# Optimization experiments

Hardware: AMD Instinct MI355X
Metric: run time of the kernel (lower is better)

The kernel has to match this reference:

```python
import jax, jax.numpy as jnp
import numpy as np

NEG_SLOPE = 0.2  # LeakyReLU slope used in the torch module


def setup_inputs() -> dict:
    key = jax.random.key(0)
    k1, k2, k3, k4 = jax.random.split(key, 4)
    B, W, K, E = 32, 128, 128, 256  # E = 2*window_size (gatv2 doubles embed_dim)
    x = jax.random.normal(k1, (B, W, K), dtype=jnp.float32)
    lin_w = jax.random.normal(k2, (E, 2 * W), dtype=jnp.float32) * 0.05
    lin_b = jnp.zeros((E,), dtype=jnp.float32)
    a = jax.random.normal(k3, (E, 1), dtype=jnp.float32) * 0.1
    bias = jax.random.normal(k4, (K, K), dtype=jnp.float32) * 0.1
    return {"x": x, "lin_w": lin_w, "lin_b": lin_b, "a": a, "bias": bias}


def reference(x, lin_w, lin_b, a, bias):
    # x: [B, window, K] -> permute to [B, K, window]
    xp = jnp.transpose(x, (0, 2, 1))
    Wd = xp.shape[-1]
    # lin(concat(v_i, v_j)) = v_i @ Wl^T + v_j @ Wr^T + b, avoiding the
    # explicit repeat_interleave/repeat/cat of the torch code (same math).
    Wl, Wr = lin_w[:, :Wd], lin_w[:, Wd:]
    left = jnp.einsum('bkw,ew->bke', xp, Wl)   # [B, K, E]
    right = jnp.einsum('bkw,ew->bke', xp, Wr)  # [B, K, E]
    h = left[:, :, None, :] + right[:, None, :, :] + lin_b  # [B, K, K, E]
    h = jnp.where(h >= 0, h, NEG_SLOPE * h)  # LeakyReLU(0.2)
    e = jnp.einsum('bije,eo->bij', h, a)     # matmul with a, squeeze -> [B, K, K]
    e = e + bias                             # use_bias=True
    att = jax.nn.softmax(e, axis=2)          # dropout=0 / eval -> identity
    out = jax.nn.sigmoid(jnp.einsum('bij,bjw->biw', att, xp))  # [B, K, W]
    return jnp.transpose(out, (0, 2, 1))     # [B, window, K]
```

## Files before the change

### kernel.cpp

```cpp
#include <hip/hip_runtime.h>


typedef float v2f __attribute__((ext_vector_type(2)));
typedef float v4f __attribute__((ext_vector_type(4)));
typedef short bf16x8 __attribute__((ext_vector_type(8)));

#define WS_A6  2097152
#define WS_A4  (2097152 + 256)

__device__ __forceinline__ unsigned pack_bf16x2(float a, float b) {
    unsigned ua = __builtin_bit_cast(unsigned, a);
    unsigned ub = __builtin_bit_cast(unsigned, b);
    ua = (ua + 0x7FFFu + ((ua >> 16) & 1u)) >> 16;
    ub = (ub + 0x7FFFu + ((ub >> 16) & 1u)) >> 16;
    return ua | (ub << 16);
}

__global__ __launch_bounds__(256) void k_linear(
    const float* __restrict__ x, const float* __restrict__ lin_w,
    const float* __restrict__ lin_b, const float* __restrict__ a,
    float* __restrict__ ws)
{
    __shared__ unsigned short xT[128 * 136];
    __shared__ unsigned short As[64 * 136];

    const int t = threadIdx.x;
    const int b = blockIdx.x, rt = blockIdx.y;
    const bool isL = (rt < 4);

    if (b == 0 && rt == 0) {
        float av = a[t];
        ws[WS_A6 + t] = 0.6f * av;
        ws[WS_A4 + t] = 0.4f * av;
    }

    {
        const float* xg = x + b * 16384;
        #pragma unroll
        for (int q = 0; q < 8; ++q) {
            const int idx = t + q * 256;
            const int wp = idx >> 5;
            const int k4 = (idx & 31) << 2;
            const v4f r0 = *(const v4f*)(xg + (2 * wp) * 128 + k4);
            const v4f r1 = *(const v4f*)(xg + (2 * wp + 1) * 128 + k4);
            const int g   = wp >> 2;
            const int off = (2 * wp) & 7;
            #pragma unroll
            for (int u = 0; u < 4; ++u) {
                const int k = k4 + u;
                const int gs = g ^ ((k >> 3) & 15);
                *(unsigned*)&xT[k * 136 + (gs << 3) + off] = pack_bf16x2(r0[u], r1[u]);
            }
        }
    }
    {
        #pragma unroll
        for (int q = 0; q < 16; ++q) {
            const int idx = t + q * 256;
            const int rr = idx >> 6, wp2 = idx & 63;
            const int r = rt * 64 + rr;
            const float* Ag = isL ? (lin_w + (size_t)r * 256)
                                  : (lin_w + (size_t)(r - 256) * 256 + 128);
            const v2f wv = *(const v2f*)(Ag + 2 * wp2);
            *(unsigned*)&As[rr * 136 + 2 * wp2] = pack_bf16x2(wv.x, wv.y);
        }
    }
    __syncthreads();

    const int l = t & 63, wave = t >> 6;
    const int m0 = wave * 16;
    const int lr = l & 15, lg = l >> 4;

    bf16x8 af[4];
    #pragma unroll
    for (int kc = 0; kc < 4; ++kc)
        af[kc] = *(const bf16x8*)&As[(m0 + lr) * 136 + kc * 32 + lg * 8];

    v4f acc[8];
    #pragma unroll
    for (int nf = 0; nf < 8; ++nf) acc[nf] = (v4f){0.f, 0.f, 0.f, 0.f};

    #pragma unroll
    for (int nf = 0; nf < 8; ++nf) {
        const int row = nf * 16 + lr;
        const int vr = (row >> 3) & 15;
        #pragma unroll
        for (int kc = 0; kc < 4; ++kc) {
            const int g = kc * 4 + lg;
            const bf16x8 bfv = *(const bf16x8*)&xT[row * 136 + ((g ^ vr) << 3)];
            acc[nf] = __builtin_amdgcn_mfma_f32_16x16x32_bf16(af[kc], bfv, acc[nf], 0, 0, 0);
        }
    }

    const int rb = rt * 64 + m0 + lg * 4;
    #pragma unroll
    for (int j = 0; j < 4; ++j) {
        const float lb = isL ? lin_b[rb + j] : 0.f;
        float* dst = ws + (size_t)(b * 512 + rb + j) * 128;
        #pragma unroll
        for (int nf = 0; nf < 8; ++nf)
            dst[nf * 16 + lr] = acc[nf][j] + lb;
    }
}

__global__ __launch_bounds__(256, 1) void k_attn(
    const float* __restrict__ x, const float* __restrict__ bias,
    const float* __restrict__ ws, float* __restrict__ out)
{
    __shared__ float Rs[2][8192];
    __shared__ float Lt[256 * 16];
    __shared__ float att[16 * 132];
    __shared__ float as6[256], as4[256];

    const int t = threadIdx.x;
    const int b = blockIdx.x, it = blockIdx.y;
    const float* Pb = ws + (size_t)b * 65536;
    const float* Rsrc = Pb + 32768;

    v4f rx[8];
#define RLOAD(n_) do { const float* s_ = Rsrc + (n_) * 8192 + t * 4;  \
    _Pragma("unroll") for (int q = 0; q < 8; ++q)                     \
      rx[q] = *(const v4f*)(s_ + q * 1024); } while (0)

    RLOAD(0);

    {
        const float* Ls = Pb + it * 16;
        #pragma unroll
        for (int q = 0; q < 4; ++q) {
            const int idx = t + q * 256;
            const int e = idx >> 2, il4 = (idx & 3) * 4;
            *(v4f*)&Lt[e * 16 + il4] = *(const v4f*)(Ls + e * 128 + il4);
        }
    }
    as6[t] = ws[WS_A6 + t];
    as4[t] = ws[WS_A4 + t];

    const int jp = t & 31, iq = t >> 5;
    const int j0 = jp * 4, il0 = iq * 2;

    float acc0[4] = {}, acc1[4] = {};
    float dr[4] = {};
    float dl0 = 0.f, dl1 = 0.f;

    #pragma unroll 1
    for (int n = 0; n < 4; ++n) {
        float* rs = &Rs[n & 1][0];
        {
            float* d_ = rs + t * 4;
            #pragma unroll
            for (int q = 0; q < 8; ++q) *(v4f*)(d_ + q * 1024) = rx[q];
        }
        if (n < 3) RLOAD(n + 1);
        __syncthreads();

        const int eg0 = n * 64;
        #pragma unroll
        for (int g = 0; g < 16; ++g) {
            const int e0 = g * 4, eg = eg0 + e0;
            v4f rv[4]; float2 lv[4];
            #pragma unroll
            for (int u = 0; u < 4; ++u) {
                rv[u] = *(const v4f*)&rs[(e0 + u) * 128 + j0];
                lv[u] = *(const float2*)&Lt[(eg + u) * 16 + il0];
            }
            const v4f a6v = *(const v4f*)&as6[eg];
            const v4f a4v = *(const v4f*)&as4[eg];
            #pragma unroll
            for (int u = 0; u < 4; ++u) {
                const float a6u = a6v[u], a4u = a4v[u];
                const float l0 = lv[u].x, l1 = lv[u].y;
                dl0 = fmaf(a6u, l0, dl0);
                dl1 = fmaf(a6u, l1, dl1);
                #pragma unroll
                for (int jj = 0; jj < 4; ++jj) {
                    const float r = rv[u][jj];
                    dr[jj]   = fmaf(a6u, r, dr[jj]);
                    acc0[jj] = fmaf(a4u, fabsf(l0 + r), acc0[jj]);
                    acc1[jj] = fmaf(a4u, fabsf(l1 + r), acc1[jj]);
                }
            }
        }
    }
    __syncthreads();

    float* xT = &Rs[0][0];
    {
        const float* xg = x + b * 16384;
        #pragma unroll
        for (int q = 0; q < 16; ++q) {
            const int idx = t + q * 256;
            const int w = idx >> 5, j4 = (idx & 31) * 4;
            const int s = ((j4 >> 2) & 15) << 1;
            const v4f xv = *(const v4f*)(xg + w * 128 + j4);
            xT[(j4 + 0) * 128 + (w ^ s)] = xv[0];
            xT[(j4 + 1) * 128 + (w ^ s)] = xv[1];
            xT[(j4 + 2) * 128 + (w ^ s)] = xv[2];
            xT[(j4 + 3) * 128 + (w ^ s)] = xv[3];
        }
    }

    const int i0r = it * 16 + il0;
    float ev0[4], ev1[4];
    {
        const v4f b0 = *(const v4f*)(bias + (i0r + 0) * 128 + j0);
        const v4f b1 = *(const v4f*)(bias + (i0r + 1) * 128 + j0);
        #pragma unroll
        for (int jj = 0; jj < 4; ++jj) {
            ev0[jj] = acc0[jj] + dl0 + dr[jj] + b0[jj];
            ev1[jj] = acc1[jj] + dl1 + dr[jj] + b1[jj];
        }
    }
#define SOFTMAX_ROW(EV, ROW) do {                                               \
    float m_ = fmaxf(fmaxf(EV[0], EV[1]), fmaxf(EV[2], EV[3]));                 \
    _Pragma("unroll") for (int d_ = 1; d_ <= 16; d_ <<= 1)                      \
        m_ = fmaxf(m_, __shfl_xor(m_, d_));                                     \
    float p0 = __expf(EV[0] - m_), p1 = __expf(EV[1] - m_);                     \
    float p2 = __expf(EV[2] - m_), p3 = __expf(EV[3] - m_);                     \
    float s_ = p0 + p1 + p2 + p3;                                               \
    _Pragma("unroll") for (int d_ = 1; d_ <= 16; d_ <<= 1)                      \
        s_ += __shfl_xor(s_, d_);                                               \
    const float inv_ = 1.f / s_;                                                \
    *(v4f*)&att[(ROW) * 132 + j0] =                                             \
        (v4f){p0 * inv_, p1 * inv_, p2 * inv_, p3 * inv_}; } while (0)

    SOFTMAX_ROW(ev0, il0 + 0);
    SOFTMAX_ROW(ev1, il0 + 1);
    __syncthreads();

    const int iq2 = t & 3, wp = t >> 2;
    const int i4 = iq2 * 4, w0 = wp * 2;
    float o[2][4] = {};
    #pragma unroll 4
    for (int jc = 0; jc < 32; ++jc) {
        const int wx = w0 ^ ((jc & 15) << 1);
        v4f av[4]; v2f xv[4];
        #pragma unroll
        for (int q = 0; q < 4; ++q)
            av[q] = *(const v4f*)&att[(i4 + q) * 132 + jc * 4];
        #pragma unroll
        for (int u = 0; u < 4; ++u)
            xv[u] = *(const v2f*)&xT[(jc * 4 + u) * 128 + wx];
        #pragma unroll
        for (int u = 0; u < 4; ++u)
            #pragma unroll
            for (int q = 0; q < 4; ++q) {
                o[0][q] = fmaf(xv[u].x, av[q][u], o[0][q]);
                o[1][q] = fmaf(xv[u].y, av[q][u], o[1][q]);
            }
    }
    #pragma unroll
    for (int w = 0; w < 2; ++w) {
        v4f r;
        r[0] = 1.f / (1.f + __expf(-o[w][0]));
        r[1] = 1.f / (1.f + __expf(-o[w][1]));
        r[2] = 1.f / (1.f + __expf(-o[w][2]));
        r[3] = 1.f / (1.f + __expf(-o[w][3]));
        *(v4f*)(out + (size_t)b * 16384 + (w0 + w) * 128 + it * 16 + i4) = r;
    }
}

extern "C" void kernel_launch(void* const* d_in, const int* in_sizes, int n_in,
                              void* d_out, int out_size, void* d_ws, size_t ws_size,
                              hipStream_t stream) {
    const float* x     = (const float*)d_in[0];
    const float* lin_w = (const float*)d_in[1];
    const float* lin_b = (const float*)d_in[2];
    const float* a     = (const float*)d_in[3];
    const float* bias  = (const float*)d_in[4];
    float* ws  = (float*)d_ws;
    float* out = (float*)d_out;

    k_linear<<<dim3(32, 8), 256, 0, stream>>>(x, lin_w, lin_b, a, ws);
    k_attn  <<<dim3(32, 8), 256, 0, stream>>>(x, bias, ws, out);
}
```

Measured before the change: 33.68 us.

## Fuse linear projection into attention kernel, recomputing projections per block in LDS

New measurement: 36.77 us. 1.09x slower.

```diff
diff --git a/kernel.cpp b/kernel.cpp
--- a/kernel.cpp
+++ b/kernel.cpp
@@ -4,9 +4,6 @@
 typedef float v2f __attribute__((ext_vector_type(2)));
 typedef float v4f __attribute__((ext_vector_type(4)));
 typedef short bf16x8 __attribute__((ext_vector_type(8)));
-
-#define WS_A6  2097152
-#define WS_A4  (2097152 + 256)
 
 __device__ __forceinline__ unsigned pack_bf16x2(float a, float b) {
     unsigned ua = __builtin_bit_cast(unsigned, a);
@@ -15,24 +12,25 @@
     ub = (ub + 0x7FFFu + ((ub >> 16) & 1u)) >> 16;
     return ua | (ub << 16);
 }
-
-__global__ __launch_bounds__(256) void k_linear(
+__device__ __forceinline__ float bf2f(unsigned h) {
+    unsigned u = h << 16;
+    return __builtin_bit_cast(float, u);
+}
+
+__global__ __launch_bounds__(256) void k_fused(
     const float* __restrict__ x, const float* __restrict__ lin_w,
     const float* __restrict__ lin_b, const float* __restrict__ a,
-    float* __restrict__ ws)
+    const float* __restrict__ bias, float* __restrict__ out)
 {
     __shared__ unsigned short xT[128 * 136];
-    __shared__ unsigned short As[64 * 136];
+    __shared__ unsigned short As2[64 * 264];
+    __shared__ float Rs[64 * 132];
+    __shared__ float Lt[256 * 18];
+    __shared__ float att[16 * 132];
+    __shared__ float as6[256], as4[256];
 
     const int t = threadIdx.x;
-    const int b = blockIdx.x, rt = blockIdx.y;
-    const bool isL = (rt < 4);
-
-    if (b == 0 && rt == 0) {
-        float av = a[t];
-        ws[WS_A6 + t] = 0.6f * av;
-        ws[WS_A4 + t] = 0.4f * av;
-    }
+    const int b = blockIdx.x, it = blockIdx.y;
 
     {
         const float* xg = x + b * 16384;
@@ -53,89 +51,11 @@
             }
         }
     }
-    {
-        #pragma unroll
-        for (int q = 0; q < 16; ++q) {
-            const int idx = t + q * 256;
-            const int rr = idx >> 6, wp2 = idx & 63;
-            const int r = rt * 64 + rr;
-            const float* Ag = isL ? (lin_w + (size_t)r * 256)
-                                  : (lin_w + (size_t)(r - 256) * 256 + 128);
-            const v2f wv = *(const v2f*)(Ag + 2 * wp2);
-            *(unsigned*)&As[rr * 136 + 2 * wp2] = pack_bf16x2(wv.x, wv.y);
-        }
-    }
-    __syncthreads();
+    as6[t] = 0.6f * a[t];
+    as4[t] = 0.4f * a[t];
 
     const int l = t & 63, wave = t >> 6;
-    const int m0 = wave * 16;
     const int lr = l & 15, lg = l >> 4;
-
-    bf16x8 af[4];
-    #pragma unroll
-    for (int kc = 0; kc < 4; ++kc)
-        af[kc] = *(const bf16x8*)&As[(m0 + lr) * 136 + kc * 32 + lg * 8];
-
-    v4f acc[8];
-    #pragma unroll
-    for (int nf = 0; nf < 8; ++nf) acc[nf] = (v4f){0.f, 0.f, 0.f, 0.f};
-
-    #pragma unroll
-    for (int nf = 0; nf < 8; ++nf) {
-        const int row = nf * 16 + lr;
-        const int vr = (row >> 3) & 15;
-        #pragma unroll
-        for (int kc = 0; kc < 4; ++kc) {
-            const int g = kc * 4 + lg;
-            const bf16x8 bfv = *(const bf16x8*)&xT[row * 136 + ((g ^ vr) << 3)];
-            acc[nf] = __builtin_amdgcn_mfma_f32_16x16x32_bf16(af[kc], bfv, acc[nf], 0, 0, 0);
-        }
-    }
-
-    const int rb = rt * 64 + m0 + lg * 4;
-    #pragma unroll
-    for (int j = 0; j < 4; ++j) {
-        const float lb = isL ? lin_b[rb + j] : 0.f;
-        float* dst = ws + (size_t)(b * 512 + rb + j) * 128;
-        #pragma unroll
-        for (int nf = 0; nf < 8; ++nf)
-            dst[nf * 16 + lr] = acc[nf][j] + lb;
-    }
-}
-
-__global__ __launch_bounds__(256, 1) void k_attn(
-    const float* __restrict__ x, const float* __restrict__ bias,
-    const float* __restrict__ ws, float* __restrict__ out)
-{
-    __shared__ float Rs[2][8192];
-    __shared__ float Lt[256 * 16];
-    __shared__ float att[16 * 132];
-    __shared__ float as6[256], as4[256];
-
-    const int t = threadIdx.x;
-    const int b = blockIdx.x, it = blockIdx.y;
-    const float* Pb = ws + (size_t)b * 65536;
-    const float* Rsrc = Pb + 32768;
-
-    v4f rx[8];
-#define RLOAD(n_) do { const float* s_ = Rsrc + (n_) * 8192 + t * 4;  \
-    _Pragma("unroll") for (int q = 0; q < 8; ++q)                     \
-      rx[q] = *(const v4f*)(s_ + q * 1024); } while (0)
-
-    RLOAD(0);
-
-    {
-        const float* Ls = Pb + it * 16;
-        #pragma unroll
-        for (int q = 0; q < 4; ++q) {
-            const int idx = t + q * 256;
-            const int e = idx >> 2, il4 = (idx & 3) * 4;
-            *(v4f*)&Lt[e * 16 + il4] = *(const v4f*)(Ls + e * 128 + il4);
-        }
-    }
-    as6[t] = ws[WS_A6 + t];
-    as4[t] = ws[WS_A4 + t];
-
     const int jp = t & 31, iq = t >> 5;
     const int j0 = jp * 4, il0 = iq * 2;
 
@@ -144,25 +64,66 @@
     float dl0 = 0.f, dl1 = 0.f;
 
     #pragma unroll 1
-    for (int n = 0; n < 4; ++n) {
-        float* rs = &Rs[n & 1][0];
+    for (int c = 0; c < 4; ++c) {
+        #pragma unroll
+        for (int q = 0; q < 32; ++q) {
+            const int idx = t + q * 256;
+            const int rr = idx >> 7, cp = idx & 127;
+            const v2f wv = *(const v2f*)(lin_w + (size_t)(c * 64 + rr) * 256 + 2 * cp);
+            *(unsigned*)&As2[rr * 264 + 2 * cp] = pack_bf16x2(wv.x, wv.y);
+        }
+        __syncthreads();
+
         {
-            float* d_ = rs + t * 4;
-            #pragma unroll
-            for (int q = 0; q < 8; ++q) *(v4f*)(d_ + q * 1024) = rx[q];
-        }
-        if (n < 3) RLOAD(n + 1);
+            bf16x8 afL[4], afR[4];
+            #pragma unroll
+            for (int kc = 0; kc < 4; ++kc) {
+                afL[kc] = *(const bf16x8*)&As2[(wave * 16 + lr) * 264 + kc * 32 + lg * 8];
+                afR[kc] = *(const bf16x8*)&As2[(wave * 16 + lr) * 264 + 128 + kc * 32 + lg * 8];
+            }
+            v4f accL = (v4f){0.f, 0.f, 0.f, 0.f};
+            {
+                const int row = it * 16 + lr;
+                const int vr = (row >> 3) & 15;
+                #pragma unroll
+                for (int kc = 0; kc < 4; ++kc) {
+                    const bf16x8 bfv = *(const bf16x8*)&xT[row * 136 + (((kc * 4 + lg) ^ vr) << 3)];
+                    accL = __builtin_amdgcn_mfma_f32_16x16x32_bf16(afL[kc], bfv, accL, 0, 0, 0);
+                }
+            }
+            v4f accR[8];
+            #pragma unroll
+            for (int nf = 0; nf < 8; ++nf) accR[nf] = (v4f){0.f, 0.f, 0.f, 0.f};
+            #pragma unroll
+            for (int nf = 0; nf < 8; ++nf) {
+                const int row = nf * 16 + lr;
+                const int vr = (row >> 3) & 15;
+                #pragma unroll
+                for (int kc = 0; kc < 4; ++kc) {
+                    const bf16x8 bfv = *(const bf16x8*)&xT[row * 136 + (((kc * 4 + lg) ^ vr) << 3)];
+                    accR[nf] = __builtin_amdgcn_mfma_f32_16x16x32_bf16(afR[kc], bfv, accR[nf], 0, 0, 0);
+                }
+            }
+            const int el = wave * 16 + lg * 4;
+            #pragma unroll
+            for (int j = 0; j < 4; ++j) {
+                Lt[(c * 64 + el + j) * 18 + lr] = accL[j] + lin_b[c * 64 + el + j];
+                #pragma unroll
+                for (int nf = 0; nf < 8; ++nf)
+                    Rs[(el + j) * 132 + nf * 16 + lr] = accR[nf][j];
+            }
+        }
         __syncthreads();
 
-        const int eg0 = n * 64;
+        const int eg0 = c * 64;
         #pragma unroll
         for (int g = 0; g < 16; ++g) {
             const int e0 = g * 4, eg = eg0 + e0;
             v4f rv[4]; float2 lv[4];
             #pragma unroll
             for (int u = 0; u < 4; ++u) {
-                rv[u] = *(const v4f*)&rs[(e0 + u) * 128 + j0];
-                lv[u] = *(const float2*)&Lt[(eg + u) * 16 + il0];
+                rv[u] = *(const v4f*)&Rs[(e0 + u) * 132 + j0];
+                lv[u] = *(const float2*)&Lt[(eg + u) * 18 + il0];
             }
             const v4f a6v = *(const v4f*)&as6[eg];
             const v4f a4v = *(const v4f*)&as4[eg];
@@ -181,23 +142,7 @@
                 }
             }
         }
-    }
-    __syncthreads();
-
-    float* xT = &Rs[0][0];
-    {
-        const float* xg = x + b * 16384;
-        #pragma unroll
-        for (int q = 0; q < 16; ++q) {
-            const int idx = t + q * 256;
-            const int w = idx >> 5, j4 = (idx & 31) * 4;
-            const int s = ((j4 >> 2) & 15) << 1;
-            const v4f xv = *(const v4f*)(xg + w * 128 + j4);
-            xT[(j4 + 0) * 128 + (w ^ s)] = xv[0];
-            xT[(j4 + 1) * 128 + (w ^ s)] = xv[1];
-            xT[(j4 + 2) * 128 + (w ^ s)] = xv[2];
-            xT[(j4 + 3) * 128 + (w ^ s)] = xv[3];
-        }
+        __syncthreads();
     }
 
     const int i0r = it * 16 + il0;
@@ -230,23 +175,29 @@
 
     const int iq2 = t & 3, wp = t >> 2;
     const int i4 = iq2 * 4, w0 = wp * 2;
+    const int g2 = w0 >> 3, off2 = w0 & 7;
     float o[2][4] = {};
     #pragma unroll 4
     for (int jc = 0; jc < 32; ++jc) {
-        const int wx = w0 ^ ((jc & 15) << 1);
-        v4f av[4]; v2f xv[4];
+        v4f av[4];
         #pragma unroll
         for (int q = 0; q < 4; ++q)
             av[q] = *(const v4f*)&att[(i4 + q) * 132 + jc * 4];
+        float xv0[4], xv1[4];
+        #pragma unroll
+        for (int u = 0; u < 4; ++u) {
+            const int k = jc * 4 + u;
+            const int gs = g2 ^ ((k >> 3) & 15);
+            const unsigned pp = *(const unsigned*)&xT[k * 136 + (gs << 3) + off2];
+            xv0[u] = bf2f(pp & 0xFFFFu);
+            xv1[u] = bf2f(pp >> 16);
+        }
         #pragma unroll
         for (int u = 0; u < 4; ++u)
-            xv[u] = *(const v2f*)&xT[(jc * 4 + u) * 128 + wx];
-        #pragma unroll
-        for (int u = 0; u < 4; ++u)
             #pragma unroll
             for (int q = 0; q < 4; ++q) {
-                o[0][q] = fmaf(xv[u].x, av[q][u], o[0][q]);
-                o[1][q] = fmaf(xv[u].y, av[q][u], o[1][q]);
+                o[0][q] = fmaf(xv0[u], av[q][u], o[0][q]);
+                o[1][q] = fmaf(xv1[u], av[q][u], o[1][q]);
             }
     }
     #pragma unroll
@@ -268,9 +219,8 @@
     const float* lin_b = (const float*)d_in[2];
     const float* a     = (const float*)d_in[3];
     const float* bias  = (const float*)d_in[4];
-    float* ws  = (float*)d_ws;
     float* out = (float*)d_out;
-
-    k_linear<<<dim3(32, 8), 256, 0, stream>>>(x, lin_w, lin_b, a, ws);
-    k_attn  <<<dim3(32, 8), 256, 0, stream>>>(x, bias, ws, out);
-}
+    (void)d_ws; (void)ws_size;
+
+    k_fused<<<dim3(32, 8), 256, 0, stream>>>(x, lin_w, lin_b, a, bias, out);
+}
```

## Split linear kernel over K halves, load weights directly, coalesce output via LDS

Applied to the files above, without the earlier changes.

New measurement: 32.48 us. -3.6%, faster.

```diff
diff --git a/kernel.cpp b/kernel.cpp
--- a/kernel.cpp
+++ b/kernel.cpp
@@ -21,85 +21,86 @@
     const float* __restrict__ lin_b, const float* __restrict__ a,
     float* __restrict__ ws)
 {
-    __shared__ unsigned short xT[128 * 136];
-    __shared__ unsigned short As[64 * 136];
+    __shared__ unsigned short xT[64 * 136];
+    __shared__ float Ps[64 * 68];
 
     const int t = threadIdx.x;
-    const int b = blockIdx.x, rt = blockIdx.y;
+    const int b = blockIdx.x, rt = blockIdx.y, kt = blockIdx.z;
+    const int r0 = rt * 64, k0 = kt * 64;
     const bool isL = (rt < 4);
 
-    if (b == 0 && rt == 0) {
+    if (b == 0 && rt == 0 && kt == 0) {
         float av = a[t];
         ws[WS_A6 + t] = 0.6f * av;
         ws[WS_A4 + t] = 0.4f * av;
     }
 
     {
-        const float* xg = x + b * 16384;
-        #pragma unroll
-        for (int q = 0; q < 8; ++q) {
+        const float* xg = x + b * 16384 + k0;
+        #pragma unroll
+        for (int q = 0; q < 4; ++q) {
             const int idx = t + q * 256;
-            const int wp = idx >> 5;
-            const int k4 = (idx & 31) << 2;
-            const v4f r0 = *(const v4f*)(xg + (2 * wp) * 128 + k4);
-            const v4f r1 = *(const v4f*)(xg + (2 * wp + 1) * 128 + k4);
+            const int wp = idx >> 4;
+            const int k4 = (idx & 15) << 2;
+            const v4f r0v = *(const v4f*)(xg + (2 * wp) * 128 + k4);
+            const v4f r1v = *(const v4f*)(xg + (2 * wp + 1) * 128 + k4);
             const int g   = wp >> 2;
             const int off = (2 * wp) & 7;
             #pragma unroll
             for (int u = 0; u < 4; ++u) {
-                const int k = k4 + u;
-                const int gs = g ^ ((k >> 3) & 15);
-                *(unsigned*)&xT[k * 136 + (gs << 3) + off] = pack_bf16x2(r0[u], r1[u]);
-            }
-        }
-    }
-    {
-        #pragma unroll
-        for (int q = 0; q < 16; ++q) {
-            const int idx = t + q * 256;
-            const int rr = idx >> 6, wp2 = idx & 63;
-            const int r = rt * 64 + rr;
-            const float* Ag = isL ? (lin_w + (size_t)r * 256)
-                                  : (lin_w + (size_t)(r - 256) * 256 + 128);
-            const v2f wv = *(const v2f*)(Ag + 2 * wp2);
-            *(unsigned*)&As[rr * 136 + 2 * wp2] = pack_bf16x2(wv.x, wv.y);
+                const int kk = k4 + u;
+                const int gs = g ^ ((kk >> 3) & 15);
+                *(unsigned*)&xT[kk * 136 + (gs << 3) + off] = pack_bf16x2(r0v[u], r1v[u]);
+            }
         }
     }
     __syncthreads();
 
     const int l = t & 63, wave = t >> 6;
-    const int m0 = wave * 16;
     const int lr = l & 15, lg = l >> 4;
-
+    const int rr_a = wave * 16 + lr;
+    const int r_g  = r0 + rr_a;
+    const float* Arow = isL ? (lin_w + (size_t)r_g * 256)
+                            : (lin_w + (size_t)(r_g - 256) * 256 + 128);
     bf16x8 af[4];
     #pragma unroll
-    for (int kc = 0; kc < 4; ++kc)
-        af[kc] = *(const bf16x8*)&As[(m0 + lr) * 136 + kc * 32 + lg * 8];
-
-    v4f acc[8];
-    #pragma unroll
-    for (int nf = 0; nf < 8; ++nf) acc[nf] = (v4f){0.f, 0.f, 0.f, 0.f};
-
-    #pragma unroll
-    for (int nf = 0; nf < 8; ++nf) {
-        const int row = nf * 16 + lr;
-        const int vr = (row >> 3) & 15;
+    for (int kc = 0; kc < 4; ++kc) {
+        const v4f a0 = *(const v4f*)(Arow + kc * 32 + lg * 8);
+        const v4f a1 = *(const v4f*)(Arow + kc * 32 + lg * 8 + 4);
+        unsigned p0 = pack_bf16x2(a0[0], a0[1]), p1 = pack_bf16x2(a0[2], a0[3]);
+        unsigned p2 = pack_bf16x2(a1[0], a1[1]), p3 = pack_bf16x2(a1[2], a1[3]);
+        af[kc] = __builtin_bit_cast(bf16x8, (uint4){p0, p1, p2, p3});
+    }
+
+    v4f acc[4];
+    #pragma unroll
+    for (int nf = 0; nf < 4; ++nf) acc[nf] = (v4f){0.f, 0.f, 0.f, 0.f};
+    #pragma unroll
+    for (int nf = 0; nf < 4; ++nf) {
+        const int kk = nf * 16 + lr;
+        const int vr = (kk >> 3) & 15;
         #pragma unroll
         for (int kc = 0; kc < 4; ++kc) {
-            const int g = kc * 4 + lg;
-            const bf16x8 bfv = *(const bf16x8*)&xT[row * 136 + ((g ^ vr) << 3)];
+            const bf16x8 bfv = *(const bf16x8*)&xT[kk * 136 + (((kc * 4 + lg) ^ vr) << 3)];
             acc[nf] = __builtin_amdgcn_mfma_f32_16x16x32_bf16(af[kc], bfv, acc[nf], 0, 0, 0);
         }
     }
 
-    const int rb = rt * 64 + m0 + lg * 4;
-    #pragma unroll
-    for (int j = 0; j < 4; ++j) {
-        const float lb = isL ? lin_b[rb + j] : 0.f;
-        float* dst = ws + (size_t)(b * 512 + rb + j) * 128;
-        #pragma unroll
-        for (int nf = 0; nf < 8; ++nf)
-            dst[nf * 16 + lr] = acc[nf][j] + lb;
+    #pragma unroll
+    for (int nf = 0; nf < 4; ++nf)
+        #pragma unroll
+        for (int j = 0; j < 4; ++j)
+            Ps[(wave * 16 + lg * 4 + j) * 68 + nf * 16 + lr] = acc[nf][j];
+    __syncthreads();
+
+    #pragma unroll
+    for (int q = 0; q < 4; ++q) {
+        const int idx = t + q * 256;
+        const int rr = idx >> 4, k4 = (idx & 15) << 2;
+        const float lb = isL ? lin_b[r0 + rr] : 0.f;
+        const v4f v = *(const v4f*)&Ps[rr * 68 + k4];
+        float* dst = ws + ((size_t)(b * 512 + r0 + rr) * 128 + k0 + k4);
+        *(v4f*)dst = (v4f){v[0] + lb, v[1] + lb, v[2] + lb, v[3] + lb};
     }
 }
 
@@ -271,6 +272,6 @@
     float* ws  = (float*)d_ws;
     float* out = (float*)d_out;
 
-    k_linear<<<dim3(32, 8), 256, 0, stream>>>(x, lin_w, lin_b, a, ws);
+    k_linear<<<dim3(32, 8, 2), 256, 0, stream>>>(x, lin_w, lin_b, a, ws);
     k_attn  <<<dim3(32, 8), 256, 0, stream>>>(x, bias, ws, out);
 }
```
